# Performance work log

Measured on AMD Instinct MI355X. Metric: run time of the kernel, lower is better.

The kernel has to match this reference:

```python
import jax, jax.numpy as jnp
import numpy as np

NEG_INF = -1e20  # the repo defines INF = 1e20
TOPK = 10


def setup_inputs() -> dict:
    key = jax.random.key(0)
    k1, k2 = jax.random.split(key)
    B, N, D, H = 8, 2048, 512, 512
    context = jax.random.normal(k1, (B, N, D), dtype=jnp.float32)
    ctx_mask = jnp.ones((B, N), dtype=jnp.int32)  # all positions valid
    W = jax.random.normal(k2, (H, D), dtype=jnp.float32) * 0.02  # linear_sim weight
    return {"context": context, "W": W, "ctx_mask": ctx_mask}


def reference(context, W, ctx_mask):
    # context_fc = relu(linear_sim(context))        : [B, N, H]
    ctx_fc = jax.nn.relu(jnp.einsum('bnd,hd->bnh', context, W))
    # attention = context_fc @ context_fc^T         : [B, N, N]
    att = jnp.einsum('bnh,bmh->bnm', ctx_fc, ctx_fc)
    # masked_fill where ctx_mask == 0 (both row and column)
    m = ctx_mask.astype(bool)
    att = jnp.where(m[:, None, :], att, NEG_INF)
    att = jnp.where(m[:, :, None], att, NEG_INF)
    # build_knn_neighbourhood: keep top-k per row, everything else -INF
    k = min(TOPK, att.shape[-1])
    knn_val, knn_ind = jax.lax.top_k(att, k)  # [B, N, k]
    B, N, _ = att.shape
    bi = jnp.arange(B)[:, None, None]
    ri = jnp.arange(N)[None, :, None]
    adj = jnp.full(att.shape, NEG_INF, dtype=att.dtype).at[bi, ri, knn_ind].set(knn_val)
    return adj
```

## Files before the change

kernel.cpp:

```cpp
#include <hip/hip_runtime.h>
#include <hip/hip_bf16.h>

#define NEG_INF -1e20f

typedef __bf16 bf16x8 __attribute__((ext_vector_type(8)));
typedef float  f32x4  __attribute__((ext_vector_type(4)));

__device__ inline unsigned short f2bf(float x) {
    unsigned u = __float_as_uint(x);
    unsigned r = u + 0x7fffu + ((u >> 16) & 1u);
    return (unsigned short)(r >> 16);
}
__device__ inline float bf2f(unsigned short h) {
    return __uint_as_float((unsigned)h << 16);
}
__device__ inline unsigned fkey(float f) {
    unsigned u = __float_as_uint(f);
    return (u & 0x80000000u) ? ~u : (u | 0x80000000u);
}

__global__ __launch_bounds__(256) void split3_all(
        const float* __restrict__ ctx, const float* __restrict__ W,
        unsigned short* __restrict__ C1, unsigned short* __restrict__ C2,
        unsigned short* __restrict__ C3, unsigned short* __restrict__ W1,
        unsigned short* __restrict__ W2, unsigned short* __restrict__ W3) {
    const int b = blockIdx.x;
    const int t = threadIdx.x;
    const float* src;
    unsigned short *p1, *p2, *p3;
    int base;
    if (b < 2048) { src = ctx; p1 = C1; p2 = C2; p3 = C3; base = b * 1024; }
    else          { src = W;   p1 = W1; p2 = W2; p3 = W3; base = (b - 2048) * 1024; }
#pragma unroll
    for (int it = 0; it < 4; ++it) {
        int i = base + it * 256 + t;
        float4 v = ((const float4*)src)[i];
        ushort4 a, bb, c;
        float r;
        a.x = f2bf(v.x); r = v.x - bf2f(a.x); bb.x = f2bf(r); c.x = f2bf(r - bf2f(bb.x));
        a.y = f2bf(v.y); r = v.y - bf2f(a.y); bb.y = f2bf(r); c.y = f2bf(r - bf2f(bb.y));
        a.z = f2bf(v.z); r = v.z - bf2f(a.z); bb.z = f2bf(r); c.z = f2bf(r - bf2f(bb.z));
        a.w = f2bf(v.w); r = v.w - bf2f(a.w); bb.w = f2bf(r); c.w = f2bf(r - bf2f(bb.w));
        ((ushort4*)p1)[i] = a;
        ((ushort4*)p2)[i] = bb;
        ((ushort4*)p3)[i] = c;
    }
}

__global__ __launch_bounds__(256, 2) void fc_mfma6(
        const unsigned short* __restrict__ A1, const unsigned short* __restrict__ A2,
        const unsigned short* __restrict__ A3, const unsigned short* __restrict__ B1,
        const unsigned short* __restrict__ B2, const unsigned short* __restrict__ B3,
        unsigned short* __restrict__ Fhi, unsigned short* __restrict__ Flo) {
    __shared__ char lds[49152];

    const int t     = threadIdx.x;
    const int mBase = blockIdx.x * 128;
    const int hBase = blockIdx.y * 128;
    const int w = t >> 6, lane = t & 63;
    const int q = lane >> 4, ln = lane & 15;
    const int wn = (w >> 1) * 64;
    const int wm = (w & 1) * 64;

    f32x4 acc[4][4] = {};

    for (int kt = 0; kt < 512; kt += 32) {
#pragma unroll
        for (int p = 0; p < 3; ++p) {
            const unsigned short* pl = (p == 0) ? A1 : (p == 1) ? A2 : A3;
#pragma unroll
            for (int rr = 0; rr < 2; ++rr) {
                int chunk = rr * 256 + t;
                int row   = chunk >> 2;
                int c     = (chunk & 3) ^ ((row >> 1) & 3);
                const unsigned short* g = pl + ((size_t)(mBase + row) * 512 + kt + c * 8);
                char* l = lds + p * 8192 + chunk * 16;
                __builtin_amdgcn_global_load_lds(
                    (const __attribute__((address_space(1))) void*)g,
                    (__attribute__((address_space(3))) void*)l, 16, 0, 0);
            }
        }
#pragma unroll
        for (int p = 0; p < 3; ++p) {
            const unsigned short* pl = (p == 0) ? B1 : (p == 1) ? B2 : B3;
#pragma unroll
            for (int rr = 0; rr < 2; ++rr) {
                int chunk = rr * 256 + t;
                int row   = chunk >> 2;
                int c     = (chunk & 3) ^ ((row >> 1) & 3);
                const unsigned short* g = pl + ((size_t)(hBase + row) * 512 + kt + c * 8);
                char* l = lds + 24576 + p * 8192 + chunk * 16;
                __builtin_amdgcn_global_load_lds(
                    (const __attribute__((address_space(1))) void*)g,
                    (__attribute__((address_space(3))) void*)l, 16, 0, 0);
            }
        }
        __syncthreads();

        bf16x8 a1[4], a2[4], a3[4], b1[4], b2[4], b3[4];
#pragma unroll
        for (int i = 0; i < 4; ++i) {
            int mA = wn + i * 16 + ln;
            int oA = (mA * 4 + (q ^ ((mA >> 1) & 3))) * 16;
            a1[i] = *(const bf16x8*)(lds +     0 + oA);
            a2[i] = *(const bf16x8*)(lds +  8192 + oA);
            a3[i] = *(const bf16x8*)(lds + 16384 + oA);
            int mB = wm + i * 16 + ln;
            int oB = (mB * 4 + (q ^ ((mB >> 1) & 3))) * 16;
            b1[i] = *(const bf16x8*)(lds + 24576 + oB);
            b2[i] = *(const bf16x8*)(lds + 32768 + oB);
            b3[i] = *(const bf16x8*)(lds + 40960 + oB);
        }
#pragma unroll
        for (int i = 0; i < 4; ++i)
#pragma unroll
            for (int j = 0; j < 4; ++j) {
                acc[i][j] = __builtin_amdgcn_mfma_f32_16x16x32_bf16(a1[i], b1[j], acc[i][j], 0, 0, 0);
                acc[i][j] = __builtin_amdgcn_mfma_f32_16x16x32_bf16(a1[i], b2[j], acc[i][j], 0, 0, 0);
                acc[i][j] = __builtin_amdgcn_mfma_f32_16x16x32_bf16(a2[i], b1[j], acc[i][j], 0, 0, 0);
                acc[i][j] = __builtin_amdgcn_mfma_f32_16x16x32_bf16(a2[i], b2[j], acc[i][j], 0, 0, 0);
                acc[i][j] = __builtin_amdgcn_mfma_f32_16x16x32_bf16(a1[i], b3[j], acc[i][j], 0, 0, 0);
                acc[i][j] = __builtin_amdgcn_mfma_f32_16x16x32_bf16(a3[i], b1[j], acc[i][j], 0, 0, 0);
            }
        __syncthreads();
    }

    unsigned* tb = (unsigned*)(lds + w * 4352);
    const int rg = lane >> 4;
    const int c4 = lane & 15;
#pragma unroll
    for (int i = 0; i < 4; ++i) {
#pragma unroll
        for (int j = 0; j < 4; ++j)
#pragma unroll
            for (int r = 0; r < 4; ++r) {
                float v = fmaxf(acc[i][j][r], 0.f);
                unsigned short hi = f2bf(v);
                unsigned short lo = f2bf(v - bf2f(hi));
                tb[(q * 4 + r) * 68 + j * 16 + ln] =
                    (unsigned)hi | ((unsigned)lo << 16);
            }
#pragma unroll
        for (int it = 0; it < 4; ++it) {
            int row = it * 4 + rg;
            uint4 pk = *(const uint4*)&tb[row * 68 + c4 * 4];
            ushort4 h, l;
            h.x = (unsigned short)pk.x; l.x = (unsigned short)(pk.x >> 16);
            h.y = (unsigned short)pk.y; l.y = (unsigned short)(pk.y >> 16);
            h.z = (unsigned short)pk.z; l.z = (unsigned short)(pk.z >> 16);
            h.w = (unsigned short)pk.w; l.w = (unsigned short)(pk.w >> 16);
            size_t off = (size_t)(mBase + wn + i * 16 + row) * 512 + hBase + wm + c4 * 4;
            *(ushort4*)(Fhi + off) = h;
            *(ushort4*)(Flo + off) = l;
        }
    }
}

__global__ __launch_bounds__(256, 2) void att_mfma_sym(
        const unsigned short* __restrict__ Fhi, const unsigned short* __restrict__ Flo,
        const int* __restrict__ mask, float* __restrict__ out) {
    __shared__ char lds[32768];

    const int t = threadIdx.x;
    const int b = blockIdx.z;
    int p = blockIdx.x, ti = 0;
    while (p >= 16 - ti) { p -= 16 - ti; ++ti; }
    const int tj = ti + p;
    const int nBase = ti * 128;
    const int mBase = tj * 128;
    const int w    = t >> 6, lane = t & 63;
    const int q    = lane >> 4, ln = lane & 15;
    const int wn   = (w >> 1) * 64;
    const int wm   = (w & 1) * 64;
    const size_t rowB = (size_t)b * 2048;

    f32x4 acc[4][4] = {};

    for (int kt = 0; kt < 512; kt += 32) {
#pragma unroll
        for (int pp = 0; pp < 4; ++pp) {
            const unsigned short* plane = (pp & 1) ? Flo : Fhi;
            int rbase = (pp < 2) ? nBase : mBase;
#pragma unroll
            for (int r = 0; r < 2; ++r) {
                int chunk = r * 256 + t;
                int row   = chunk >> 2;
                int c     = (chunk & 3) ^ ((row >> 1) & 3);
                const unsigned short* g =
                    plane + ((rowB + rbase + row) * 512 + kt + c * 8);
                char* l = lds + pp * 8192 + chunk * 16;
                __builtin_amdgcn_global_load_lds(
                    (const __attribute__((address_space(1))) void*)g,
                    (__attribute__((address_space(3))) void*)l, 16, 0, 0);
            }
        }
        __syncthreads();

        bf16x8 ah[4], al[4], bh[4], bl[4];
#pragma unroll
        for (int i = 0; i < 4; ++i) {
            int mA = wn + i * 16 + ln;
            int oA = (mA * 4 + (q ^ ((mA >> 1) & 3))) * 16;
            ah[i] = *(const bf16x8*)(lds +     0 + oA);
            al[i] = *(const bf16x8*)(lds +  8192 + oA);
            int mB = wm + i * 16 + ln;
            int oB = (mB * 4 + (q ^ ((mB >> 1) & 3))) * 16;
            bh[i] = *(const bf16x8*)(lds + 16384 + oB);
            bl[i] = *(const bf16x8*)(lds + 24576 + oB);
        }
#pragma unroll
        for (int i = 0; i < 4; ++i)
#pragma unroll
            for (int j = 0; j < 4; ++j) {
                acc[i][j] = __builtin_amdgcn_mfma_f32_16x16x32_bf16(ah[i], bh[j], acc[i][j], 0, 0, 0);
                acc[i][j] = __builtin_amdgcn_mfma_f32_16x16x32_bf16(ah[i], bl[j], acc[i][j], 0, 0, 0);
                acc[i][j] = __builtin_amdgcn_mfma_f32_16x16x32_bf16(al[i], bh[j], acc[i][j], 0, 0, 0);
            }
        __syncthreads();
    }

    const int* mb = mask + b * 2048;
    float* outB = out + (size_t)b * 2048 * 2048;
    int cm[4];
#pragma unroll
    for (int j = 0; j < 4; ++j) cm[j] = mb[mBase + wm + j * 16 + ln];

    float* tb = (float*)(lds + w * 4352);
    const int rg = lane >> 4;
    const int c4 = lane & 15;
    const bool mirror = (ti != tj);
#pragma unroll
    for (int i = 0; i < 4; ++i) {
        int n0 = nBase + wn + i * 16;
        int rmv[4];
#pragma unroll
        for (int r = 0; r < 4; ++r) rmv[r] = mb[n0 + q * 4 + r];
#pragma unroll
        for (int j = 0; j < 4; ++j)
#pragma unroll
            for (int r = 0; r < 4; ++r) {
                float v = ((rmv[r] != 0) & (cm[j] != 0)) ? acc[i][j][r] : NEG_INF;
                tb[(q * 4 + r) * 68 + j * 16 + ln] = v;
            }
#pragma unroll
        for (int it = 0; it < 4; ++it) {
            int row = it * 4 + rg;
            float4 vv = *(const float4*)&tb[row * 68 + c4 * 4];
            *(float4*)(outB + (size_t)(n0 + row) * 2048 + mBase + wm + c4 * 4) = vv;
        }
        if (mirror) {
#pragma unroll
            for (int ps = 0; ps < 4; ++ps) {
                float4 mv;
                mv.x = tb[(ps * 4 + 0) * 68 + lane];
                mv.y = tb[(ps * 4 + 1) * 68 + lane];
                mv.z = tb[(ps * 4 + 2) * 68 + lane];
                mv.w = tb[(ps * 4 + 3) * 68 + lane];
                *(float4*)(outB + (size_t)(mBase + wm + lane) * 2048 + n0 + ps * 4) = mv;
            }
        }
    }
}

__global__ __launch_bounds__(256) void topk_rows(float* __restrict__ att) {
    __shared__ float patch[2048];
    __shared__ unsigned long long cand[40];
    __shared__ int   top_i[10];
    __shared__ float top_v[10];

    const int t    = threadIdx.x;
    const int lane = t & 63;
    const int w    = t >> 6;
    float* row = att + (size_t)blockIdx.x * 2048;

    float4 a = ((const float4*)row)[2 * t];
    float4 c = ((const float4*)row)[2 * t + 1];
    float v[8] = {a.x, a.y, a.z, a.w, c.x, c.y, c.z, c.w};

    unsigned key[8];
#pragma unroll
    for (int j = 0; j < 8; ++j) key[j] = fkey(v[j]);

    unsigned lk = key[0]; int lj = 0;
#pragma unroll
    for (int j = 1; j < 8; ++j)
        if (key[j] > lk) { lk = key[j]; lj = j; }

    for (int r = 0; r < 10; ++r) {
        unsigned M = lk;
#pragma unroll
        for (int off = 1; off < 64; off <<= 1) {
            unsigned o = __shfl_xor(M, off, 64);
            M = (o > M) ? o : M;
        }
        unsigned long long ball = __ballot(lk == M);
        int src  = __ffsll(ball) - 1;
        int widx = __shfl(t * 8 + lj, src, 64);
        if (lane == 0)
            cand[w * 10 + r] =
                ((unsigned long long)M << 32) | (unsigned)(~(unsigned)widx);
        if (lane == src) {
            key[lj] = 0u;
            lk = key[0]; lj = 0;
#pragma unroll
            for (int j = 1; j < 8; ++j)
                if (key[j] > lk) { lk = key[j]; lj = j; }
        }
    }
    __syncthreads();

    if (w == 0) {
        unsigned long long k2 = (lane < 40) ? cand[lane] : 0ull;
        for (int r = 0; r < 10; ++r) {
            unsigned long long m = k2;
#pragma unroll
            for (int off = 1; off < 64; off <<= 1) {
                unsigned long long o = __shfl_xor(m, off, 64);
                m = (o > m) ? o : m;
            }
            if (lane == r) {
                unsigned hu = (unsigned)(m >> 32);
                unsigned fu = (hu & 0x80000000u) ? (hu ^ 0x80000000u) : ~hu;
                top_v[r] = __uint_as_float(fu);
                top_i[r] = (int)(~(unsigned)(m & 0xffffffffu));
            }
            if (k2 == m) k2 = 0ull;
        }
    }

    float4 ninf4 = make_float4(NEG_INF, NEG_INF, NEG_INF, NEG_INF);
    ((float4*)patch)[2 * t]     = ninf4;
    ((float4*)patch)[2 * t + 1] = ninf4;
    __syncthreads();
    if (t < 10) patch[top_i[t]] = top_v[t];
    __syncthreads();
    ((float4*)row)[2 * t]     = ((float4*)patch)[2 * t];
    ((float4*)row)[2 * t + 1] = ((float4*)patch)[2 * t + 1];
}

extern "C" void kernel_launch(void* const* d_in, const int* in_sizes, int n_in,
                              void* d_out, int out_size, void* d_ws, size_t ws_size,
                              hipStream_t stream) {
    const float* ctx  = (const float*)d_in[0];
    const float* W    = (const float*)d_in[1];
    const int*   mask = (const int*)d_in[2];
    float* out = (float*)d_out;

    const size_t CN = (size_t)16384 * 512;
    const size_t WN = (size_t)512 * 512;
    unsigned short* C1 = (unsigned short*)d_out;
    unsigned short* C2 = C1 + CN;
    unsigned short* C3 = C2 + CN;
    unsigned short* W1 = C3 + CN;
    unsigned short* W2 = W1 + WN;
    unsigned short* W3 = W2 + WN;

    unsigned short* Fhi = (unsigned short*)d_ws;
    unsigned short* Flo = Fhi + CN;

    dim3 blk(256);
    split3_all<<<dim3(2112), blk, 0, stream>>>(ctx, W, C1, C2, C3, W1, W2, W3);
    fc_mfma6<<<dim3(128, 4), blk, 0, stream>>>(C1, C2, C3, W1, W2, W3, Fhi, Flo);
    att_mfma_sym<<<dim3(136, 1, 8), blk, 0, stream>>>(Fhi, Flo, mask, out);
    topk_rows<<<dim3(16384), blk, 0, stream>>>(out);
}
```

Measured before the change: 366.5 us.

## Replace per-wave top-10 rounds with threshold filter from per-thread maxima

Instead of running ten shuffle-reduction rounds in each of the four waves, each thread publishes its local max. One wave then selects the 10th largest of those 256 maxima as a threshold. Elements at or above the threshold are compacted into a candidate list with shared atomics, and one wave runs the final top-10 over the candidates. This cuts the reduction work in three of the four waves but adds extra barriers, a serial wave-0 phase and an atomic compaction step, and it truncates at 512 candidates if many values tie.

```diff
diff --git a/kernel.cpp b/kernel.cpp
--- a/kernel.cpp
+++ b/kernel.cpp
@@ -264,7 +264,10 @@
 
 __global__ __launch_bounds__(256) void topk_rows(float* __restrict__ att) {
     __shared__ float patch[2048];
-    __shared__ unsigned long long cand[40];
+    __shared__ unsigned long long tmax[256];
+    __shared__ unsigned long long cand[512];
+    __shared__ int   ncand;
+    __shared__ unsigned m10key;
     __shared__ int   top_i[10];
     __shared__ float top_v[10];
 
@@ -281,38 +284,70 @@
 #pragma unroll
     for (int j = 0; j < 8; ++j) key[j] = fkey(v[j]);
 
-    unsigned lk = key[0]; int lj = 0;
-#pragma unroll
-    for (int j = 1; j < 8; ++j)
-        if (key[j] > lk) { lk = key[j]; lj = j; }
-
-    for (int r = 0; r < 10; ++r) {
-        unsigned M = lk;
-#pragma unroll
-        for (int off = 1; off < 64; off <<= 1) {
-            unsigned o = __shfl_xor(M, off, 64);
-            M = (o > M) ? o : M;
-        }
-        unsigned long long ball = __ballot(lk == M);
-        int src  = __ffsll(ball) - 1;
-        int widx = __shfl(t * 8 + lj, src, 64);
-        if (lane == 0)
-            cand[w * 10 + r] =
-                ((unsigned long long)M << 32) | (unsigned)(~(unsigned)widx);
-        if (lane == src) {
-            key[lj] = 0u;
-            lk = key[0]; lj = 0;
-#pragma unroll
-            for (int j = 1; j < 8; ++j)
-                if (key[j] > lk) { lk = key[j]; lj = j; }
-        }
-    }
+    unsigned lmax = key[0];
+#pragma unroll
+    for (int j = 1; j < 8; ++j) lmax = (key[j] > lmax) ? key[j] : lmax;
+    tmax[t] = ((unsigned long long)lmax << 32) | (unsigned)(~(unsigned)t);
+    if (t == 0) ncand = 0;
     __syncthreads();
 
     if (w == 0) {
-        unsigned long long k2 = (lane < 40) ? cand[lane] : 0ull;
+        unsigned long long k[4];
+#pragma unroll
+        for (int s = 0; s < 4; ++s) k[s] = tmax[s * 64 + lane];
+        unsigned long long lk = k[0]; int li = 0;
+#pragma unroll
+        for (int s = 1; s < 4; ++s)
+            if (k[s] > lk) { lk = k[s]; li = s; }
+        unsigned long long m = 0;
         for (int r = 0; r < 10; ++r) {
-            unsigned long long m = k2;
+            m = lk;
+#pragma unroll
+            for (int off = 1; off < 64; off <<= 1) {
+                unsigned long long o = __shfl_xor(m, off, 64);
+                m = (o > m) ? o : m;
+            }
+            if (lk == m) {
+                k[li] = 0ull;
+                lk = k[0]; li = 0;
+#pragma unroll
+                for (int s = 1; s < 4; ++s)
+                    if (k[s] > lk) { lk = k[s]; li = s; }
+            }
+        }
+        if (lane == 0) m10key = (unsigned)(m >> 32);
+    }
+    __syncthreads();
+
+    const unsigned T = m10key;
+    int cnt = 0;
+    unsigned long long mine[8];
+#pragma unroll
+    for (int j = 0; j < 8; ++j)
+        if (key[j] >= T)
+            mine[cnt++] = ((unsigned long long)key[j] << 32) |
+                          (unsigned)(~(unsigned)(t * 8 + j));
+    if (cnt) {
+        int slot = atomicAdd(&ncand, cnt);
+        for (int i = 0; i < cnt; ++i)
+            if (slot + i < 512) cand[slot + i] = mine[i];
+    }
+    __syncthreads();
+    const int nc = (ncand < 512) ? ncand : 512;
+
+    if (w == 0) {
+        unsigned long long k[8];
+#pragma unroll
+        for (int s = 0; s < 8; ++s) {
+            int idx = s * 64 + lane;
+            k[s] = (idx < nc) ? cand[idx] : 0ull;
+        }
+        unsigned long long lk = k[0]; int li = 0;
+#pragma unroll
+        for (int s = 1; s < 8; ++s)
+            if (k[s] > lk) { lk = k[s]; li = s; }
+        for (int r = 0; r < 10; ++r) {
+            unsigned long long m = lk;
 #pragma unroll
             for (int off = 1; off < 64; off <<= 1) {
                 unsigned long long o = __shfl_xor(m, off, 64);
@@ -324,7 +359,13 @@
                 top_v[r] = __uint_as_float(fu);
                 top_i[r] = (int)(~(unsigned)(m & 0xffffffffu));
             }
-            if (k2 == m) k2 = 0ull;
+            if (lk == m) {
+                k[li] = 0ull;
+                lk = k[0]; li = 0;
+#pragma unroll
+                for (int s = 1; s < 8; ++s)
+                    if (k[s] > lk) { lk = k[s]; li = s; }
+            }
         }
     }
 
```

Result: slower. 381.6 us (+4.1%).

## Process one top-k row per wavefront with cached second-best candidate

Applied to the files above, without the earlier changes.

The top-k kernel now gives each 64-lane wavefront a whole 2048-element row (32 values per lane) instead of one row per 256-thread block. This removes the cross-wave candidate merge and the block-wide barriers. Each lane also keeps its best and second-best keys, so a full rescan of its 32 registers is only needed after both have been taken. The cost is higher register pressure from 32 keys per lane, and the global loads are now strided per lane (lane*32), which may coalesce less well.

```diff
diff --git a/kernel.cpp b/kernel.cpp
--- a/kernel.cpp
+++ b/kernel.cpp
@@ -263,79 +263,76 @@
 }
 
 __global__ __launch_bounds__(256) void topk_rows(float* __restrict__ att) {
-    __shared__ float patch[2048];
-    __shared__ unsigned long long cand[40];
-    __shared__ int   top_i[10];
-    __shared__ float top_v[10];
+    __shared__ float patch[4][2048];
 
     const int t    = threadIdx.x;
+    const int w    = t >> 6;
     const int lane = t & 63;
-    const int w    = t >> 6;
-    float* row = att + (size_t)blockIdx.x * 2048;
-
-    float4 a = ((const float4*)row)[2 * t];
-    float4 c = ((const float4*)row)[2 * t + 1];
-    float v[8] = {a.x, a.y, a.z, a.w, c.x, c.y, c.z, c.w};
-
-    unsigned key[8];
-#pragma unroll
-    for (int j = 0; j < 8; ++j) key[j] = fkey(v[j]);
-
-    unsigned lk = key[0]; int lj = 0;
-#pragma unroll
-    for (int j = 1; j < 8; ++j)
-        if (key[j] > lk) { lk = key[j]; lj = j; }
-
+    float* row = att + ((size_t)blockIdx.x * 4 + w) * 2048;
+
+    unsigned key[32];
+#pragma unroll
+    for (int s = 0; s < 8; ++s) {
+        float4 v = *(const float4*)(row + lane * 32 + s * 4);
+        key[s * 4 + 0] = fkey(v.x);
+        key[s * 4 + 1] = fkey(v.y);
+        key[s * 4 + 2] = fkey(v.z);
+        key[s * 4 + 3] = fkey(v.w);
+    }
+
+    unsigned h1 = key[0]; int i1 = 0;
+#pragma unroll
+    for (int j = 1; j < 32; ++j)
+        if (key[j] > h1) { h1 = key[j]; i1 = j; }
+    unsigned h2 = 0; int i2 = 0;
+#pragma unroll
+    for (int j = 0; j < 32; ++j) {
+        bool ok = (j != i1) && (key[j] > h2);
+        h2 = ok ? key[j] : h2;
+        i2 = ok ? j : i2;
+    }
+    bool h2valid = true;
+    unsigned taken = 0;
+
+    unsigned myk = 0; int myidx = 0;
     for (int r = 0; r < 10; ++r) {
-        unsigned M = lk;
+        unsigned M = h1;
 #pragma unroll
         for (int off = 1; off < 64; off <<= 1) {
             unsigned o = __shfl_xor(M, off, 64);
             M = (o > M) ? o : M;
         }
-        unsigned long long ball = __ballot(lk == M);
+        unsigned long long ball = __ballot(h1 == M);
         int src  = __ffsll(ball) - 1;
-        int widx = __shfl(t * 8 + lj, src, 64);
-        if (lane == 0)
-            cand[w * 10 + r] =
-                ((unsigned long long)M << 32) | (unsigned)(~(unsigned)widx);
+        int wloc = __shfl(i1, src, 64);
+        if (lane == r) { myk = M; myidx = src * 32 + wloc; }
         if (lane == src) {
-            key[lj] = 0u;
-            lk = key[0]; lj = 0;
-#pragma unroll
-            for (int j = 1; j < 8; ++j)
-                if (key[j] > lk) { lk = key[j]; lj = j; }
-        }
-    }
-    __syncthreads();
-
-    if (w == 0) {
-        unsigned long long k2 = (lane < 40) ? cand[lane] : 0ull;
-        for (int r = 0; r < 10; ++r) {
-            unsigned long long m = k2;
-#pragma unroll
-            for (int off = 1; off < 64; off <<= 1) {
-                unsigned long long o = __shfl_xor(m, off, 64);
-                m = (o > m) ? o : m;
-            }
-            if (lane == r) {
-                unsigned hu = (unsigned)(m >> 32);
-                unsigned fu = (hu & 0x80000000u) ? (hu ^ 0x80000000u) : ~hu;
-                top_v[r] = __uint_as_float(fu);
-                top_i[r] = (int)(~(unsigned)(m & 0xffffffffu));
-            }
-            if (k2 == m) k2 = 0ull;
-        }
-    }
-
+            taken |= 1u << i1;
+            if (h2valid) { h1 = h2; i1 = i2; h2valid = false; }
+            else {
+                unsigned bh = 0; int bi = 0;
+#pragma unroll
+                for (int j = 0; j < 32; ++j) {
+                    bool ok = (((taken >> j) & 1u) == 0u) && (key[j] > bh);
+                    bh = ok ? key[j] : bh;
+                    bi = ok ? j : bi;
+                }
+                h1 = bh; i1 = bi;
+            }
+        }
+    }
+
+    float* pw = patch[w];
     float4 ninf4 = make_float4(NEG_INF, NEG_INF, NEG_INF, NEG_INF);
-    ((float4*)patch)[2 * t]     = ninf4;
-    ((float4*)patch)[2 * t + 1] = ninf4;
-    __syncthreads();
-    if (t < 10) patch[top_i[t]] = top_v[t];
-    __syncthreads();
-    ((float4*)row)[2 * t]     = ((float4*)patch)[2 * t];
-    ((float4*)row)[2 * t + 1] = ((float4*)patch)[2 * t + 1];
+#pragma unroll
+    for (int s = 0; s < 8; ++s) ((float4*)pw)[s * 64 + lane] = ninf4;
+    if (lane < 10) {
+        unsigned fu = (myk & 0x80000000u) ? (myk ^ 0x80000000u) : ~myk;
+        pw[myidx] = __uint_as_float(fu);
+    }
+#pragma unroll
+    for (int s = 0; s < 8; ++s)
+        ((float4*)row)[s * 64 + lane] = ((float4*)pw)[s * 64 + lane];
 }
 
 extern "C" void kernel_launch(void* const* d_in, const int* in_sizes, int n_in,
@@ -362,5 +359,5 @@
     split3_all<<<dim3(2112), blk, 0, stream>>>(ctx, W, C1, C2, C3, W1, W2, W3);
     fc_mfma6<<<dim3(128, 4), blk, 0, stream>>>(C1, C2, C3, W1, W2, W3, Fhi, Flo);
     att_mfma_sym<<<dim3(136, 1, 8), blk, 0, stream>>>(Fhi, Flo, mask, out);
-    topk_rows<<<dim3(16384), blk, 0, stream>>>(out);
-}
+    topk_rows<<<dim3(4096), blk, 0, stream>>>(out);
+}
```

Measured after the change: 319.3 us. 1.15x faster.
